# Kernel optimization log

Measured on AMD Instinct MI355X. Metric: run time of the kernel, lower is better.

## Reference

```python
import jax, jax.numpy as jnp
import numpy as np

B, S, D, H = 2, 2048, 1024, 16
HD = D // H  # head_dim = 64


def setup_inputs() -> dict:
    key = jax.random.key(0)
    ks = jax.random.split(key, 6)
    scale = 0.02
    x = jax.random.normal(ks[0], (B, S, D), dtype=jnp.float32)
    Wq = jax.random.normal(ks[1], (D, D), dtype=jnp.float32) * scale
    Wk = jax.random.normal(ks[2], (D, D), dtype=jnp.float32) * scale
    Wv = jax.random.normal(ks[3], (D, D), dtype=jnp.float32) * scale
    Wo = jax.random.normal(ks[4], (D, D), dtype=jnp.float32) * scale
    bo = jnp.zeros((D,), dtype=jnp.float32)
    return {"x": x, "Wq": Wq, "Wk": Wk, "Wv": Wv, "Wo": Wo, "bo": bo}


def reference(x, Wq, Wk, Wv, Wo, bo):
    b, s, _ = x.shape
    # Linear projections (qkv_bias=False), split into heads: [b, h, s, hd]
    def split_heads(t):
        return t.reshape(b, s, H, HD).transpose(0, 2, 1, 3)
    q = split_heads(x @ Wq)
    k = split_heads(x @ Wk)
    v = split_heads(x @ Wv)
    # Scaled dot-product scores: [b, h, s, s]
    scores = jnp.einsum('bhqd,bhkd->bhqk', q, k) / jnp.sqrt(jnp.float32(HD))
    # Causal mask: triu(ones, diagonal=1) positions -> -inf
    causal = jnp.triu(jnp.ones((s, s), dtype=bool), k=1)
    scores = jnp.where(causal, -jnp.inf, scores)
    attn = jax.nn.softmax(scores, axis=-1)
    # dropout p=0.0 (eval-equivalent): identity
    ctx = jnp.einsum('bhqk,bhkd->bhqd', attn, v)  # [b, h, s, hd]
    ctx = ctx.transpose(0, 2, 1, 3).reshape(b, s, D)
    return ctx @ Wo + bo
```

## Files before the change

### kernel.cpp

```cpp
#include <hip/hip_runtime.h>
#include <math.h>

#define BB 2
#define SS 2048
#define DD 1024
#define HH 16
#define HD 64
#define MM (BB * SS)

typedef __bf16 bf16;
typedef __attribute__((ext_vector_type(8))) __bf16 bf16x8;
typedef __attribute__((ext_vector_type(4))) __bf16 bf16x4;
typedef __attribute__((ext_vector_type(4))) short short4v;
typedef __attribute__((ext_vector_type(4))) float f32x4;

#if __has_builtin(__builtin_amdgcn_exp2f)
#define EXP2F(x) __builtin_amdgcn_exp2f(x)
#else
#define EXP2F(x) exp2f(x)
#endif

__device__ __forceinline__ f32x4 pv_mfma16(bf16x4 a, short4v b, f32x4 c) {
    return __builtin_amdgcn_mfma_f32_16x16x16bf16_1k(
        __builtin_bit_cast(short4v, a), b, c, 0, 0, 0);
}

__device__ __forceinline__ void gld_lds16(const void* g, void* l) {
    __builtin_amdgcn_global_load_lds(
        (const __attribute__((address_space(1))) void*)g,
        (__attribute__((address_space(3))) void*)l, 16, 0, 0);
}

__global__ __launch_bounds__(256) void prep(
    const float* __restrict__ x,
    const float* __restrict__ W0, const float* __restrict__ W1,
    const float* __restrict__ W2, const float* __restrict__ W3,
    bf16* __restrict__ xb, bf16* __restrict__ Wt)
{
    __shared__ float tile[32][33];
    const int z = blockIdx.z;
    if (z < 4) {
        const float* W = (z == 0) ? W0 : (z == 1) ? W1 : (z == 2) ? W2 : W3;
        bf16* O = Wt + (size_t)z * DD * DD;
        const int tx = threadIdx.x & 31, ty = threadIdx.x >> 5;
        const int k0 = blockIdx.y * 32, n0 = blockIdx.x * 32;
#pragma unroll
        for (int i = 0; i < 4; ++i)
            tile[ty + i * 8][tx] = W[(size_t)(k0 + ty + i * 8) * DD + n0 + tx];
        __syncthreads();
#pragma unroll
        for (int i = 0; i < 4; ++i)
            O[(size_t)(n0 + ty + i * 8) * DD + k0 + tx] = (bf16)tile[tx][ty + i * 8];
    } else {
        const int lb = (z - 4) * 1024 + blockIdx.y * 32 + blockIdx.x;
        const size_t i = ((size_t)lb * 256 + threadIdx.x) * 8;
        const float4 a = *(const float4*)(x + i);
        const float4 b = *(const float4*)(x + i + 4);
        bf16x8 o;
        o[0] = (bf16)a.x; o[1] = (bf16)a.y; o[2] = (bf16)a.z; o[3] = (bf16)a.w;
        o[4] = (bf16)b.x; o[5] = (bf16)b.y; o[6] = (bf16)b.z; o[7] = (bf16)b.w;
        *(bf16x8*)(xb + i) = o;
    }
}

__device__ __forceinline__ void mfma_core(
    const bf16* __restrict__ A, const bf16* __restrict__ Bt,
    int bm, int bn, int K, bf16* As, bf16* Bs, f32x4 (&acc)[4][4])
{
    const int t = threadIdx.x;
    const int w = t >> 6;
    const int l16 = t & 15, quad = (t >> 4) & 3;
    const int wr = w >> 1, wc = w & 1;
    const int arow = t >> 2;
    const int achk = (t & 3) << 3;

    const bf16* gA = A + (size_t)(bm + arow) * K + achk;
    const bf16* gB = Bt + (size_t)(bn + arow) * K + achk;
    bf16* lA = As + w * 512;
    bf16* lB = Bs + w * 512;

    for (int k0 = 0; k0 < K; k0 += 32) {
        gld_lds16(gA + k0, lA);
        gld_lds16(gA + (size_t)64 * K + k0, lA + 2048);
        gld_lds16(gB + k0, lB);
        gld_lds16(gB + (size_t)64 * K + k0, lB + 2048);
        __syncthreads();

        bf16x8 af[4], bv[4];
#pragma unroll
        for (int i = 0; i < 4; ++i) {
            af[i] = *(const bf16x8*)(As + (wr * 64 + i * 16 + l16) * 32 + quad * 8);
            bv[i] = *(const bf16x8*)(Bs + (wc * 64 + i * 16 + l16) * 32 + quad * 8);
        }
#pragma unroll
        for (int mi = 0; mi < 4; ++mi)
#pragma unroll
            for (int ni = 0; ni < 4; ++ni)
                acc[mi][ni] = __builtin_amdgcn_mfma_f32_16x16x32_bf16(
                    af[mi], bv[ni], acc[mi][ni], 0, 0, 0);
        __syncthreads();
    }
}

__global__ __launch_bounds__(256) void gemm_qkv(
    const bf16* __restrict__ xb, const bf16* __restrict__ Wt,
    bf16* __restrict__ Qb, bf16* __restrict__ Kb, bf16* __restrict__ Vb)
{
    __shared__ __align__(16) bf16 As[128 * 32];
    __shared__ __align__(16) bf16 Bs[128 * 32];
    const int bm = blockIdx.y * 128, bn = blockIdx.x * 128, z = blockIdx.z;

    f32x4 acc[4][4] = {};
    mfma_core(xb, Wt + (size_t)z * DD * DD, bm, bn, DD, As, Bs, acc);

    const int t = threadIdx.x;
    const int w = t >> 6, l16 = t & 15, quad = (t >> 4) & 3;
    const int wr = w >> 1, wc = w & 1;
    bf16* outp = (z == 0) ? Qb : (z == 1) ? Kb : Vb;
    const float scl = (z == 0) ? 0.18033688011f : 1.0f;

#pragma unroll
    for (int mi = 0; mi < 4; ++mi) {
#pragma unroll
        for (int ni = 0; ni < 4; ++ni) {
            const int col = bn + wc * 64 + ni * 16 + l16;
            const int h = col >> 6, hd = col & 63;
#pragma unroll
            for (int r = 0; r < 4; ++r) {
                const int row = bm + wr * 64 + mi * 16 + quad * 4 + r;
                const int b = row >> 11, s = row & (SS - 1);
                size_t addr;
                if (z < 2) addr = ((size_t)((b * HH + h) * SS + s)) * HD + hd;
                else       addr = ((size_t)((b * HH + h) * HD + hd)) * SS + s;
                outp[addr] = (bf16)(acc[mi][ni][r] * scl);
            }
        }
    }
}

__global__ __launch_bounds__(256) void gemm_out(
    const bf16* __restrict__ ctx, const bf16* __restrict__ Wto,
    const float* __restrict__ bias, float* __restrict__ out)
{
    __shared__ __align__(16) bf16 As[128 * 32];
    __shared__ __align__(16) bf16 Bs[128 * 32];
    const int bm = blockIdx.y * 128, bn = blockIdx.x * 128;

    f32x4 acc[4][4] = {};
    mfma_core(ctx, Wto, bm, bn, DD, As, Bs, acc);

    const int t = threadIdx.x;
    const int w = t >> 6, l16 = t & 15, quad = (t >> 4) & 3;
    const int wr = w >> 1, wc = w & 1;

#pragma unroll
    for (int mi = 0; mi < 4; ++mi) {
#pragma unroll
        for (int ni = 0; ni < 4; ++ni) {
            const int col = bn + wc * 64 + ni * 16 + l16;
            const float b = bias[col];
#pragma unroll
            for (int r = 0; r < 4; ++r) {
                const int row = bm + wr * 64 + mi * 16 + quad * 4 + r;
                out[(size_t)row * DD + col] = acc[mi][ni][r] + b;
            }
        }
    }
}

__global__ __launch_bounds__(256, 4) void attn_flash(
    const bf16* __restrict__ Q, const bf16* __restrict__ K,
    const bf16* __restrict__ Vt, bf16* __restrict__ ctx)
{
    __shared__ __align__(16) bf16 Ks[2][64 * 64];
    __shared__ __align__(16) bf16 Vs[2][64 * 64];

    const int t = threadIdx.x;
    const int w = t >> 6;
    const int lane = t & 63;
    const int l16 = lane & 15, quad = lane >> 4;

    const int L  = blockIdx.x;
    const int bh = L & 31;
    const int idx = L >> 5;
    const int pg = idx >> 3, pr = idx & 7;
    const int qg = (pg == 0) ? 31 - pr : (pg == 1) ? pr
                 : (pg == 2) ? 23 - pr : 8 + pr;
    const int q0b = qg * 64;
    const int q0w = q0b + w * 16;
    const int qrow = q0w + l16;
    const int nkt = qg + 1;

    const bf16* Qp = Q  + ((size_t)bh * SS + q0w) * HD;
    const bf16* Kp = K  + (size_t)bh * SS * HD;
    const bf16* Vp = Vt + (size_t)bh * HD * SS;

    const bf16x8 bQ0 = *(const bf16x8*)(Qp + l16 * HD + quad * 8);
    const bf16x8 bQ1 = *(const bf16x8*)(Qp + l16 * HD + 32 + quad * 8);

    const int r8 = lane >> 3, cs = lane & 7;
    const int rowA = (w * 2) * 8 + r8, rowB = (w * 2 + 1) * 8 + r8;
    const int cA = (cs - rowA) & 7, cB = (cs - rowB) & 7;
    const bf16* gK0 = Kp + (size_t)rowA * HD + cA * 8;
    const bf16* gK1 = Kp + (size_t)rowB * HD + cB * 8;
    const bf16* gV0 = Vp + (size_t)rowA * SS + cA * 8;
    const bf16* gV1 = Vp + (size_t)rowB * SS + cB * 8;
    bf16* const lK0 = &Ks[0][(w * 2) * 512];
    bf16* const lK1 = &Ks[0][(w * 2 + 1) * 512];
    bf16* const lV0 = &Vs[0][(w * 2) * 512];
    bf16* const lV1 = &Vs[0][(w * 2 + 1) * 512];

#define STAGE(BUF, KB) do {                                              \
        gld_lds16(gK0 + (size_t)(KB) * HD, lK0 + (BUF) * 4096);          \
        gld_lds16(gK1 + (size_t)(KB) * HD, lK1 + (BUF) * 4096);          \
        gld_lds16(gV0 + (KB),              lV0 + (BUF) * 4096);          \
        gld_lds16(gV1 + (KB),              lV1 + (BUF) * 4096);          \
    } while (0)

    const int offK0 = l16 * 64 + ((quad + l16) & 7) * 8;
    const int offK1 = l16 * 64 + ((quad + 4 + l16) & 7) * 8;
    int offV[4];
#pragma unroll
    for (int mi = 0; mi < 4; ++mi)
        offV[mi] = l16 * 64 + ((((quad >> 1) + 2 * mi + l16) & 7) * 8)
                 + (quad & 1) * 4;

    const bf16* const KsB = &Ks[0][0];
    const bf16* const VsB = &Vs[0][0];

    f32x4 accO[4] = {{0,0,0,0},{0,0,0,0},{0,0,0,0},{0,0,0,0}};
    float Lr = 0.f;

#define TILE(BUF, KB) do {                                                   \
        f32x4 St[4] = {{0,0,0,0},{0,0,0,0},{0,0,0,0},{0,0,0,0}};             \
        _Pragma("unroll")                                                    \
        for (int mi = 0; mi < 4; ++mi) {                                     \
            const bf16x8 a0 = *(const bf16x8*)(KsB + (BUF) * 4096            \
                                               + mi * 1024 + offK0);         \
            const bf16x8 a1 = *(const bf16x8*)(KsB + (BUF) * 4096            \
                                               + mi * 1024 + offK1);         \
            St[mi] = __builtin_amdgcn_mfma_f32_16x16x32_bf16(                \
                a0, bQ0, St[mi], 0, 0, 0);                                   \
            St[mi] = __builtin_amdgcn_mfma_f32_16x16x32_bf16(                \
                a1, bQ1, St[mi], 0, 0, 0);                                   \
        }                                                                    \
        if ((KB) + 63 > q0w) {                                               \
            _Pragma("unroll")                                                \
            for (int mi = 0; mi < 4; ++mi)                                   \
                _Pragma("unroll")                                            \
                for (int rr = 0; rr < 4; ++rr)                               \
                    if ((KB) + mi * 16 + quad * 4 + rr > qrow)               \
                        St[mi][rr] = -1e30f;                                 \
        }                                                                    \
        float rs = 0.f;                                                      \
        short4v pb[4];                                                       \
        _Pragma("unroll")                                                    \
        for (int mi = 0; mi < 4; ++mi) {                                     \
            bf16x4 pk;                                                       \
            _Pragma("unroll")                                                \
            for (int rr = 0; rr < 4; ++rr) {                                 \
                const float p = EXP2F(St[mi][rr]);                           \
                rs += p;                                                     \
                pk[rr] = (bf16)p;                                            \
            }                                                                \
            pb[mi] = __builtin_bit_cast(short4v, pk);                        \
        }                                                                    \
        rs += __shfl_xor(rs, 16);                                            \
        rs += __shfl_xor(rs, 32);                                            \
        Lr += rs;                                                            \
        _Pragma("unroll")                                                    \
        for (int mi = 0; mi < 4; ++mi) {                                     \
            _Pragma("unroll")                                                \
            for (int db = 0; db < 4; ++db) {                                 \
                const bf16x4 aV = *(const bf16x4*)(VsB + (BUF) * 4096        \
                                                   + db * 1024 + offV[mi]);  \
                accO[db] = pv_mfma16(aV, pb[mi], accO[db]);                  \
            }                                                                \
        }                                                                    \
    } while (0)

    STAGE(0, 0);
    int kb = 0;
    for (int kt = 0; kt + 2 <= nkt; kt += 2) {
        __syncthreads();
        STAGE(1, kb + 64);
        TILE(0, kb);
        __syncthreads();
        if (kt + 2 < nkt) STAGE(0, kb + 128);
        TILE(1, kb + 64);
        kb += 128;
    }
    if (nkt & 1) {
        __syncthreads();
        TILE(0, kb);
    }
#undef TILE
#undef STAGE

    const float rinv = 1.0f / Lr;
    const int b = bh >> 4, h = bh & (HH - 1);
    bf16* op = ctx + ((size_t)(b * SS + q0w + l16)) * DD + h * HD;
#pragma unroll
    for (int db = 0; db < 4; ++db) {
        bf16x4 o;
#pragma unroll
        for (int rr = 0; rr < 4; ++rr) o[rr] = (bf16)(accO[db][rr] * rinv);
        *(bf16x4*)(op + db * 16 + quad * 4) = o;
    }
}

extern "C" void kernel_launch(void* const* d_in, const int* in_sizes, int n_in,
                              void* d_out, int out_size, void* d_ws, size_t ws_size,
                              hipStream_t stream)
{
    const float* x  = (const float*)d_in[0];
    const float* Wq = (const float*)d_in[1];
    const float* Wk = (const float*)d_in[2];
    const float* Wv = (const float*)d_in[3];
    const float* Wo = (const float*)d_in[4];
    const float* bo = (const float*)d_in[5];
    float* out = (float*)d_out;

    const size_t chunk = (size_t)MM * DD;
    bf16* xb  = (bf16*)d_ws;
    bf16* Wt  = xb + chunk;
    bf16* Qb  = Wt + 4 * (size_t)DD * DD;
    bf16* Kb  = Qb + chunk;
    bf16* Vb  = Kb + chunk;
    bf16* ctx = Vb + chunk;

    prep<<<dim3(32, 32, 6), dim3(256), 0, stream>>>(x, Wq, Wk, Wv, Wo, xb, Wt);

    gemm_qkv<<<dim3(DD / 128, MM / 128, 3), dim3(256), 0, stream>>>(xb, Wt, Qb, Kb, Vb);

    attn_flash<<<dim3(BB * HH * (SS / 64)), dim3(256), 0, stream>>>(Qb, Kb, Vb, ctx);

    gemm_out<<<dim3(DD / 128, MM / 128), dim3(256), 0, stream>>>(
        ctx, Wt + 3 * (size_t)DD * DD, bo, out);
}
```

Measured before the change: 187.2 us.

## Double-buffer GEMM LDS tiles with async prefetch and XOR-swizzle LDS layout

```diff
diff --git a/kernel.cpp b/kernel.cpp
--- a/kernel.cpp
+++ b/kernel.cpp
@@ -72,42 +72,81 @@
     const int l16 = t & 15, quad = (t >> 4) & 3;
     const int wr = w >> 1, wc = w & 1;
     const int arow = t >> 2;
-    const int achk = (t & 3) << 3;
+    const int achk = (((t & 3) ^ ((t >> 3) & 3)) << 3);
 
     const bf16* gA = A + (size_t)(bm + arow) * K + achk;
     const bf16* gB = Bt + (size_t)(bn + arow) * K + achk;
     bf16* lA = As + w * 512;
     bf16* lB = Bs + w * 512;
 
-    for (int k0 = 0; k0 < K; k0 += 32) {
-        gld_lds16(gA + k0, lA);
-        gld_lds16(gA + (size_t)64 * K + k0, lA + 2048);
-        gld_lds16(gB + k0, lB);
-        gld_lds16(gB + (size_t)64 * K + k0, lB + 2048);
-        __syncthreads();
-
-        bf16x8 af[4], bv[4];
-#pragma unroll
-        for (int i = 0; i < 4; ++i) {
-            af[i] = *(const bf16x8*)(As + (wr * 64 + i * 16 + l16) * 32 + quad * 8);
-            bv[i] = *(const bf16x8*)(Bs + (wc * 64 + i * 16 + l16) * 32 + quad * 8);
+    const int swz = (l16 >> 1) & 3;
+    int offA[4], offB[4];
+#pragma unroll
+    for (int i = 0; i < 4; ++i) {
+        offA[i] = (wr * 64 + i * 16 + l16) * 32 + ((quad ^ swz) << 3);
+        offB[i] = (wc * 64 + i * 16 + l16) * 32 + ((quad ^ swz) << 3);
+    }
+
+#define GSTAGE(BUF, KO) do {                                                  \
+        gld_lds16(gA + (KO),                  lA + (BUF) * 4096);             \
+        gld_lds16(gA + (size_t)64 * K + (KO), lA + (BUF) * 4096 + 2048);      \
+        gld_lds16(gB + (KO),                  lB + (BUF) * 4096);             \
+        gld_lds16(gB + (size_t)64 * K + (KO), lB + (BUF) * 4096 + 2048);      \
+    } while (0)
+
+#define GCOMPUTE(BUF) do {                                                    \
+        const bf16* Ab = As + (BUF) * 4096;                                   \
+        const bf16* Bb = Bs + (BUF) * 4096;                                   \
+        bf16x8 af[4], bv[4];                                                  \
+        _Pragma("unroll")                                                     \
+        for (int i = 0; i < 4; ++i) {                                         \
+            af[i] = *(const bf16x8*)(Ab + offA[i]);                           \
+            bv[i] = *(const bf16x8*)(Bb + offB[i]);                           \
+        }                                                                     \
+        _Pragma("unroll")                                                     \
+        for (int mi = 0; mi < 4; ++mi)                                        \
+            _Pragma("unroll")                                                 \
+            for (int ni = 0; ni < 4; ++ni)                                    \
+                acc[mi][ni] = __builtin_amdgcn_mfma_f32_16x16x32_bf16(        \
+                    af[mi], bv[ni], acc[mi][ni], 0, 0, 0);                    \
+    } while (0)
+
+#define GBAR() do {                                                           \
+        asm volatile("s_barrier" ::: "memory");                               \
+        __builtin_amdgcn_sched_barrier(0);                                    \
+    } while (0)
+
+    GSTAGE(0, 0);
+    const int nk = K >> 5;
+    for (int kt = 0; kt < nk; kt += 2) {
+        GSTAGE(1, (kt + 1) << 5);
+        asm volatile("s_waitcnt vmcnt(4)" ::: "memory");
+        GBAR();
+        GCOMPUTE(0);
+        asm volatile("s_waitcnt lgkmcnt(0)" ::: "memory");
+        GBAR();
+        if (kt + 2 < nk) {
+            GSTAGE(0, (kt + 2) << 5);
+            asm volatile("s_waitcnt vmcnt(4)" ::: "memory");
+        } else {
+            asm volatile("s_waitcnt vmcnt(0)" ::: "memory");
         }
-#pragma unroll
-        for (int mi = 0; mi < 4; ++mi)
-#pragma unroll
-            for (int ni = 0; ni < 4; ++ni)
-                acc[mi][ni] = __builtin_amdgcn_mfma_f32_16x16x32_bf16(
-                    af[mi], bv[ni], acc[mi][ni], 0, 0, 0);
-        __syncthreads();
-    }
+        GBAR();
+        GCOMPUTE(1);
+        asm volatile("s_waitcnt lgkmcnt(0)" ::: "memory");
+        GBAR();
+    }
+#undef GBAR
+#undef GCOMPUTE
+#undef GSTAGE
 }
 
 __global__ __launch_bounds__(256) void gemm_qkv(
     const bf16* __restrict__ xb, const bf16* __restrict__ Wt,
     bf16* __restrict__ Qb, bf16* __restrict__ Kb, bf16* __restrict__ Vb)
 {
-    __shared__ __align__(16) bf16 As[128 * 32];
-    __shared__ __align__(16) bf16 Bs[128 * 32];
+    __shared__ __align__(16) bf16 As[2 * 128 * 32];
+    __shared__ __align__(16) bf16 Bs[2 * 128 * 32];
     const int bm = blockIdx.y * 128, bn = blockIdx.x * 128, z = blockIdx.z;
 
     f32x4 acc[4][4] = {};
@@ -142,8 +181,8 @@
     const bf16* __restrict__ ctx, const bf16* __restrict__ Wto,
     const float* __restrict__ bias, float* __restrict__ out)
 {
-    __shared__ __align__(16) bf16 As[128 * 32];
-    __shared__ __align__(16) bf16 Bs[128 * 32];
+    __shared__ __align__(16) bf16 As[2 * 128 * 32];
+    __shared__ __align__(16) bf16 Bs[2 * 128 * 32];
     const int bm = blockIdx.y * 128, bn = blockIdx.x * 128;
 
     f32x4 acc[4][4] = {};
```

Measured after the change: 182.9 us. 2.3% less time.
